# Performance work log

Measured on AMD Instinct MI355X. Metric: run time of the kernel, lower is better.

The kernel has to match this reference:

```python
import jax, jax.numpy as jnp
import numpy as np

D_HEAD = 64
KV_GROUPS = 3
KSIZE = 7


def _win_idx(L, ksize):
    # NATTEN neighborhood: window centered at i, shifted to stay in-bounds.
    start = jnp.clip(jnp.arange(L) - ksize // 2, 0, L - ksize)  # [L]
    return start[:, None] + jnp.arange(ksize)[None, :]          # [L, k]


def _natten2d(q, k, v, ksize):
    # q,k,v: [n, nh, H, W, e]; q pre-scaled.
    H, W = q.shape[2], q.shape[3]
    ih = _win_idx(H, ksize)  # [H, k]
    iw = _win_idx(W, ksize)  # [W, k]
    # gather per-query key/value windows: [n, nh, H, W, k, k, e]
    kg = k[:, :, ih[:, None, :, None], iw[None, :, None, :], :]
    vg = v[:, :, ih[:, None, :, None], iw[None, :, None, :], :]
    logits = jnp.einsum('nhije,nhijabe->nhijab', q, kg)  # [n,nh,H,W,k,k]
    n_, nh = logits.shape[:2]
    a = jax.nn.softmax(logits.reshape(n_, nh, H, W, ksize * ksize), axis=-1)
    a = a.reshape(logits.shape)
    return jnp.einsum('nhijab,nhijabe->nhije', a, vg)  # [n,nh,H,W,e]


def _to_heads(p, nh, e):
    n, h, w, _ = p.shape
    return p.reshape(n, h, w, nh, e).transpose(0, 3, 1, 2, 4)  # [n,nh,h,w,e]


def setup_inputs() -> dict:
    key = jax.random.key(0)
    k1, k2, k3 = jax.random.split(key, 3)
    x = jax.random.normal(k1, (2, 32, 32, 768), dtype=jnp.float32)
    w_qkv = jax.random.normal(k2, (1280, 768), dtype=jnp.float32) * 0.02
    w_out = jax.random.normal(k3, (768, 768), dtype=jnp.float32) * 0.02
    return {"x": x, "w_qkv": w_qkv, "w_out": w_out}


def reference(x, w_qkv, w_out):
    n, H, W, d_model = x.shape
    q_heads = d_model // D_HEAD
    kv_heads = q_heads // KV_GROUPS
    qkv = x @ w_qkv.T  # [n,H,W,1280]
    q, k, v = jnp.split(
        qkv, [q_heads * D_HEAD, (q_heads + kv_heads) * D_HEAD], axis=-1)
    q = _to_heads(q, q_heads, D_HEAD)
    k = jnp.tile(_to_heads(k, kv_heads, D_HEAD), (1, KV_GROUPS, 1, 1, 1))
    v = jnp.tile(_to_heads(v, kv_heads, D_HEAD), (1, KV_GROUPS, 1, 1, 1))
    q = q / (D_HEAD ** 0.5)
    o = _natten2d(q, k, v, KSIZE)           # [n,nh,H,W,e]
    o = o.transpose(0, 2, 3, 1, 4).reshape(n, H, W, d_model)
    return o @ w_out.T
```

## Files before the change

### kernel.cpp

```cpp
#include <hip/hip_runtime.h>
#include <hip/hip_bf16.h>


typedef __attribute__((ext_vector_type(8))) __bf16 bf16x8;
typedef __attribute__((ext_vector_type(4))) float floatx4;
typedef unsigned short u16;

__device__ inline u16 f2bf(float f) {
    union { float f; unsigned u; } v; v.f = f;
    return (u16)((v.u + 0x7fff + ((v.u >> 16) & 1)) >> 16);
}

template<int MODE>
__global__ __launch_bounds__(256) void gemm_fused(
    const void* __restrict__ Ain, const float* __restrict__ Bf,
    float* __restrict__ C, u16* __restrict__ Cb, u16* __restrict__ vT,
    int N, int K)
{
    __shared__ __align__(16) u16 As[4 * 64 * 32];
    __shared__ __align__(16) u16 Bs[4 * 64 * 32];
    const int tid = threadIdx.x;
    const int lane = tid & 63;
    const int wave = tid >> 6;
    const int bm = blockIdx.y * 64;
    const int bn = blockIdx.x * 64;
    const int qr = (wave >> 1) * 32;
    const int qc = (wave & 1) * 32;

    floatx4 acc[2][2] = {};

    const bool roleA = (wave < 2);
    const int t = tid & 127;
    const int kp = t & 15;
    const int rowg = t >> 4;
    const int bx = roleA ? bm : bn;
    u16* ldst = (roleA ? As : Bs) + (kp >> 2) * 2048 + (kp & 3) * 8;
    const bool a_is_bf16 = (MODE == 0) && roleA;
    const u16*   Xb = (const u16*)Ain;
    const float* Xf = roleA ? (const float*)Ain : Bf;

    float4 rf[8][2];
    uint4  rb[8];

    auto load_step = [&](int k0) {
        if (a_is_bf16) {
            #pragma unroll
            for (int rr = 0; rr < 8; rr++)
                rb[rr] = *(const uint4*)&Xb[(size_t)(bx + rowg * 8 + rr) * K + k0 + kp * 8];
        } else {
            #pragma unroll
            for (int rr = 0; rr < 8; rr++) {
                const float* p = &Xf[(size_t)(bx + rowg * 8 + rr) * K + k0 + kp * 8];
                rf[rr][0] = *(const float4*)p;
                rf[rr][1] = *(const float4*)(p + 4);
            }
        }
    };
    auto store_step = [&]() {
        if (a_is_bf16) {
            #pragma unroll
            for (int rr = 0; rr < 8; rr++)
                *(uint4*)&ldst[(rowg * 8 + rr) * 32] = rb[rr];
        } else {
            #pragma unroll
            for (int rr = 0; rr < 8; rr++) {
                union { u16 s[8]; uint4 v; } pk;
                pk.s[0] = f2bf(rf[rr][0].x); pk.s[1] = f2bf(rf[rr][0].y);
                pk.s[2] = f2bf(rf[rr][0].z); pk.s[3] = f2bf(rf[rr][0].w);
                pk.s[4] = f2bf(rf[rr][1].x); pk.s[5] = f2bf(rf[rr][1].y);
                pk.s[6] = f2bf(rf[rr][1].z); pk.s[7] = f2bf(rf[rr][1].w);
                *(uint4*)&ldst[(rowg * 8 + rr) * 32] = pk.v;
            }
        }
    };

    const int fr = lane & 15;
    const int fk = (lane >> 4) * 8;
    const int nk = K >> 7;

    load_step(0);
    for (int it = 0; it < nk; it++) {
        store_step();
        __syncthreads();
        if (it + 1 < nk)
            load_step((it + 1) * 128);
        #pragma unroll
        for (int kc = 0; kc < 4; kc++) {
            bf16x8 af0 = *(const bf16x8*)&As[kc * 2048 + (qr +      fr) * 32 + fk];
            bf16x8 af1 = *(const bf16x8*)&As[kc * 2048 + (qr + 16 + fr) * 32 + fk];
            bf16x8 bf0 = *(const bf16x8*)&Bs[kc * 2048 + (qc +      fr) * 32 + fk];
            bf16x8 bf1 = *(const bf16x8*)&Bs[kc * 2048 + (qc + 16 + fr) * 32 + fk];
            acc[0][0] = __builtin_amdgcn_mfma_f32_16x16x32_bf16(af0, bf0, acc[0][0], 0, 0, 0);
            acc[0][1] = __builtin_amdgcn_mfma_f32_16x16x32_bf16(af0, bf1, acc[0][1], 0, 0, 0);
            acc[1][0] = __builtin_amdgcn_mfma_f32_16x16x32_bf16(af1, bf0, acc[1][0], 0, 0, 0);
            acc[1][1] = __builtin_amdgcn_mfma_f32_16x16x32_bf16(af1, bf1, acc[1][1], 0, 0, 0);
        }
        __syncthreads();
    }

    const int cr = (lane >> 4) * 4;
    const int ccol = lane & 15;
    #pragma unroll
    for (int i = 0; i < 2; i++) {
        #pragma unroll
        for (int j = 0; j < 2; j++) {
            const int row0 = bm + qr + i * 16 + cr;
            const int col  = bn + qc + j * 16 + ccol;
            if (MODE == 0) {
                #pragma unroll
                for (int r = 0; r < 4; r++)
                    C[(size_t)(row0 + r) * N + col] = acc[i][j][r];
            } else {
                if (col < 1024) {
                    #pragma unroll
                    for (int r = 0; r < 4; r++)
                        Cb[(size_t)(row0 + r) * 1024 + col] = f2bf(acc[i][j][r]);
                } else {
                    ushort4 w;
                    w.x = f2bf(acc[i][j][0]); w.y = f2bf(acc[i][j][1]);
                    w.z = f2bf(acc[i][j][2]); w.w = f2bf(acc[i][j][3]);
                    *(ushort4*)&vT[(size_t)(col - 1024) * 2048 + row0] = w;
                }
            }
        }
    }
}

__global__ __launch_bounds__(256) void natten_mfma(
    const u16* __restrict__ qkv, const u16* __restrict__ vT,
    u16* __restrict__ o)
{
    __shared__ __align__(16) u16 Ks[224 * 72];
    __shared__ __align__(16) u16 Vs[64 * 224];
    __shared__ __align__(16) u16 Pw[4 * 512];
    const int h  = blockIdx.x;
    const int tb = blockIdx.y;
    const int g  = h & 3;
    const int batch = tb >> 4;
    const int ti = ((tb >> 2) & 3) * 8;
    const int tj = (tb & 3) * 8;
    const int wu_i = min(max(ti - 3, 0), 18);
    const int wu_j = min(max(tj - 3, 0), 18);
    const int tid = threadIdx.x, lane = tid & 63, wave = tid >> 6;
    const int pixbase = batch << 10;

    for (int c = tid; c < 1792; c += 256) {
        int n = c >> 3, seg = (c & 7) * 8;
        int a = n >> 4, b = min(n & 15, 13);
        int pix = pixbase + (wu_i + a) * 32 + wu_j + b;
        *(uint4*)&Ks[n * 72 + seg] =
            *(const uint4*)&qkv[(size_t)pix * 1024 + 768 + g * 64 + seg];
    }
    {
        const int b  = lane & 15;
        const int ar = lane >> 4;
        bool vok[4]; int voff[4];
        #pragma unroll
        for (int rr = 0; rr < 4; rr++) {
            int a = ar + rr * 4;
            vok[rr]  = (a < 14) && (b < 14);
            voff[rr] = (wu_i + a) * 32 + wu_j + b;
        }
        const u16* vsrc = &vT[(size_t)(g * 64 + wave * 16) * 2048 + pixbase];
        #pragma unroll 4
        for (int dd = 0; dd < 16; dd++) {
            #pragma unroll
            for (int rr = 0; rr < 4; rr++) {
                int a = ar + rr * 4;
                if (a < 14)
                    Vs[(wave * 16 + dd) * 224 + rr * 64 + lane] =
                        vok[rr] ? vsrc[voff[rr]] : (u16)0;
            }
            vsrc += 2048;
        }
    }
    __syncthreads();

    const int fr = lane & 15;
    const int fk = (lane >> 4) * 8;

    bf16x8 aq0, aq1;
    {
        int qq = wave * 16 + fr;
        int pixq = pixbase + (ti + (qq >> 3)) * 32 + tj + (qq & 7);
        const u16* qp = &qkv[(size_t)pixq * 1024 + h * 64];
        aq0 = *(const bf16x8*)(qp + fk);
        aq1 = *(const bf16x8*)(qp + 32 + fk);
    }

    bool colok[4]; int tlo[4], thi[4];
    #pragma unroll
    for (int r = 0; r < 4; r++) {
        int qq = wave * 16 + (lane >> 4) * 4 + r;
        int qi = ti + (qq >> 3), qj = tj + (qq & 7);
        int si = min(max(qi - 3, 0), 25);
        int sj = min(max(qj - 3, 0), 25);
        colok[r] = (fr < 14) && (wu_j + fr >= sj) && (wu_j + fr <= sj + 6);
        tlo[r] = si - wu_i; thi[r] = tlo[r] + 6;
    }

    float s[14][4];
    float mx[4] = {-1e30f, -1e30f, -1e30f, -1e30f};
    #pragma unroll
    for (int t = 0; t < 14; t++) {
        bf16x8 bk0 = *(const bf16x8*)&Ks[(t * 16 + fr) * 72 + fk];
        bf16x8 bk1 = *(const bf16x8*)&Ks[(t * 16 + fr) * 72 + 32 + fk];
        floatx4 a4 = {};
        a4 = __builtin_amdgcn_mfma_f32_16x16x32_bf16(aq0, bk0, a4, 0, 0, 0);
        a4 = __builtin_amdgcn_mfma_f32_16x16x32_bf16(aq1, bk1, a4, 0, 0, 0);
        #pragma unroll
        for (int r = 0; r < 4; r++) {
            bool v = colok[r] && (t >= tlo[r]) && (t <= thi[r]);
            s[t][r] = v ? a4[r] * 0.125f : -1e30f;
            mx[r] = fmaxf(mx[r], s[t][r]);
        }
    }
    #pragma unroll
    for (int r = 0; r < 4; r++) {
        mx[r] = fmaxf(mx[r], __shfl_xor(mx[r], 1));
        mx[r] = fmaxf(mx[r], __shfl_xor(mx[r], 2));
        mx[r] = fmaxf(mx[r], __shfl_xor(mx[r], 4));
        mx[r] = fmaxf(mx[r], __shfl_xor(mx[r], 8));
    }
    float l[4] = {0.f, 0.f, 0.f, 0.f};
    #pragma unroll
    for (int t = 0; t < 14; t++)
        #pragma unroll
        for (int r = 0; r < 4; r++) {
            float p = __expf(s[t][r] - mx[r]);
            s[t][r] = p; l[r] += p;
        }
    #pragma unroll
    for (int r = 0; r < 4; r++) {
        l[r] += __shfl_xor(l[r], 1);
        l[r] += __shfl_xor(l[r], 2);
        l[r] += __shfl_xor(l[r], 4);
        l[r] += __shfl_xor(l[r], 8);
    }
    float rinv[4];
    #pragma unroll
    for (int r = 0; r < 4; r++) rinv[r] = 1.0f / l[r];

    u16* pw = &Pw[wave * 512];
    floatx4 oacc[4] = {};
    #pragma unroll
    for (int kc = 0; kc < 7; kc++) {
        #pragma unroll
        for (int tt = 0; tt < 2; tt++) {
            int t = kc * 2 + tt;
            #pragma unroll
            for (int r = 0; r < 4; r++)
                pw[((lane >> 4) * 4 + r) * 32 + tt * 16 + fr] =
                    f2bf(s[t][r] * rinv[r]);
        }
        bf16x8 bp = *(const bf16x8*)&pw[fr * 32 + fk];
        #pragma unroll
        for (int u = 0; u < 4; u++) {
            bf16x8 av = *(const bf16x8*)&Vs[(u * 16 + fr) * 224 + kc * 32 + fk];
            oacc[u] = __builtin_amdgcn_mfma_f32_16x16x32_bf16(av, bp, oacc[u], 0, 0, 0);
        }
    }

    {
        int qq = wave * 16 + fr;
        int pixq = pixbase + (ti + (qq >> 3)) * 32 + tj + (qq & 7);
        u16* op = &o[(size_t)pixq * 768 + h * 64];
        #pragma unroll
        for (int u = 0; u < 4; u++) {
            ushort4 w;
            w.x = f2bf(oacc[u][0]); w.y = f2bf(oacc[u][1]);
            w.z = f2bf(oacc[u][2]); w.w = f2bf(oacc[u][3]);
            *(ushort4*)(op + u * 16 + (lane >> 4) * 4) = w;
        }
    }
}

extern "C" void kernel_launch(void* const* d_in, const int* in_sizes, int n_in,
                              void* d_out, int out_size, void* d_ws, size_t ws_size,
                              hipStream_t stream)
{
    const float* x     = (const float*)d_in[0];
    const float* w_qkv = (const float*)d_in[1];
    const float* w_out = (const float*)d_in[2];
    float* out = (float*)d_out;

    char* ws = (char*)d_ws;
    u16* qkvb = (u16*)ws; ws += (size_t)2048 * 1024 * 2;
    u16* vTb  = (u16*)ws; ws += (size_t)256 * 2048 * 2;
    u16* ob   = (u16*)ws;

    gemm_fused<1><<<dim3(1280 / 64, 2048 / 64), dim3(256), 0, stream>>>(
        x, w_qkv, nullptr, qkvb, vTb, 1280, 768);
    natten_mfma<<<dim3(12, 32), dim3(256), 0, stream>>>(qkvb, vTb, ob);
    gemm_fused<0><<<dim3(768 / 64, 2048 / 64), dim3(256), 0, stream>>>(
        ob, w_out, out, nullptr, nullptr, 768, 768);
}
```

Measured before the change: 121.2 us.

## Rework GEMM tile loading with all-thread staging, padded LDS and direct global-to-LDS

Replaces the split-role register-prefetch loader with a scheme where all 256 threads each convert and store one 32-wide k-chunk of a row. The fp32 operands go to LDS rows padded to 40 elements to cut bank conflicts. The bf16 A operand of the output projection is copied with global_load_lds directly into LDS, and conversion uses packed bf16x2 intrinsics. The software prefetch of the next k-step into registers is dropped, so global latency is no longer overlapped with the MFMA loop within a block and must be hidden by occupancy instead.

```diff
diff --git a/kernel.cpp b/kernel.cpp
--- a/kernel.cpp
+++ b/kernel.cpp
@@ -11,14 +11,29 @@
     return (u16)((v.u + 0x7fff + ((v.u >> 16) & 1)) >> 16);
 }
 
+__device__ inline void gl_lds16(const void* g, void* l) {
+    __builtin_amdgcn_global_load_lds(
+        (const __attribute__((address_space(1))) void*)g,
+        (__attribute__((address_space(3))) void*)l, 16, 0, 0);
+}
+
+__device__ inline uint4 pack8(float4 a, float4 b) {
+    union { __hip_bfloat162 h[4]; uint4 u; } r;
+    r.h[0] = __float22bfloat162_rn(float2{a.x, a.y});
+    r.h[1] = __float22bfloat162_rn(float2{a.z, a.w});
+    r.h[2] = __float22bfloat162_rn(float2{b.x, b.y});
+    r.h[3] = __float22bfloat162_rn(float2{b.z, b.w});
+    return r.u;
+}
+
 template<int MODE>
-__global__ __launch_bounds__(256) void gemm_fused(
+__global__ __launch_bounds__(256) void gemm_nt(
     const void* __restrict__ Ain, const float* __restrict__ Bf,
     float* __restrict__ C, u16* __restrict__ Cb, u16* __restrict__ vT,
     int N, int K)
 {
-    __shared__ __align__(16) u16 As[4 * 64 * 32];
-    __shared__ __align__(16) u16 Bs[4 * 64 * 32];
+    __shared__ __align__(16) u16 As[MODE ? 4 * 2560 : 4 * 2048];
+    __shared__ __align__(16) u16 Bs[4 * 2560];
     const int tid = threadIdx.x;
     const int lane = tid & 63;
     const int wave = tid >> 6;
@@ -29,67 +44,63 @@
 
     floatx4 acc[2][2] = {};
 
-    const bool roleA = (wave < 2);
-    const int t = tid & 127;
-    const int kp = t & 15;
-    const int rowg = t >> 4;
-    const int bx = roleA ? bm : bn;
-    u16* ldst = (roleA ? As : Bs) + (kp >> 2) * 2048 + (kp & 3) * 8;
-    const bool a_is_bf16 = (MODE == 0) && roleA;
-    const u16*   Xb = (const u16*)Ain;
-    const float* Xf = roleA ? (const float*)Ain : Bf;
-
-    float4 rf[8][2];
-    uint4  rb[8];
-
-    auto load_step = [&](int k0) {
-        if (a_is_bf16) {
-            #pragma unroll
-            for (int rr = 0; rr < 8; rr++)
-                rb[rr] = *(const uint4*)&Xb[(size_t)(bx + rowg * 8 + rr) * K + k0 + kp * 8];
-        } else {
-            #pragma unroll
-            for (int rr = 0; rr < 8; rr++) {
-                const float* p = &Xf[(size_t)(bx + rowg * 8 + rr) * K + k0 + kp * 8];
-                rf[rr][0] = *(const float4*)p;
-                rf[rr][1] = *(const float4*)(p + 4);
-            }
-        }
-    };
-    auto store_step = [&]() {
-        if (a_is_bf16) {
-            #pragma unroll
-            for (int rr = 0; rr < 8; rr++)
-                *(uint4*)&ldst[(rowg * 8 + rr) * 32] = rb[rr];
-        } else {
-            #pragma unroll
-            for (int rr = 0; rr < 8; rr++) {
-                union { u16 s[8]; uint4 v; } pk;
-                pk.s[0] = f2bf(rf[rr][0].x); pk.s[1] = f2bf(rf[rr][0].y);
-                pk.s[2] = f2bf(rf[rr][0].z); pk.s[3] = f2bf(rf[rr][0].w);
-                pk.s[4] = f2bf(rf[rr][1].x); pk.s[5] = f2bf(rf[rr][1].y);
-                pk.s[6] = f2bf(rf[rr][1].z); pk.s[7] = f2bf(rf[rr][1].w);
-                *(uint4*)&ldst[(rowg * 8 + rr) * 32] = pk.v;
-            }
-        }
-    };
+    const int srow = tid >> 2;
+    const int skc  = tid & 3;
+    const float* Bsrc = Bf + (size_t)(bn + srow) * K + skc * 32;
+    u16* Bdst = &Bs[skc * 2560 + srow * 40];
+    const float* Asrc = nullptr; u16* Adst = nullptr;
+    if (MODE) {
+        Asrc = (const float*)Ain + (size_t)(bm + srow) * K + skc * 32;
+        Adst = &As[skc * 2560 + srow * 40];
+    }
+    int gA[4], lA[4];
+    if (!MODE) {
+        #pragma unroll
+        for (int i = 0; i < 4; i++) {
+            int c = wave + 4 * i, kc = c & 3, rg = c >> 2;
+            gA[i] = (bm + rg * 16 + (lane >> 2)) * K + kc * 32 + (lane & 3) * 8;
+            lA[i] = kc * 2048 + rg * 512 + lane * 8;
+        }
+    }
 
     const int fr = lane & 15;
     const int fk = (lane >> 4) * 8;
     const int nk = K >> 7;
 
-    load_step(0);
     for (int it = 0; it < nk; it++) {
-        store_step();
+        const int k0 = it * 128;
+        {
+            const float* p = Bsrc + k0;
+            #pragma unroll
+            for (int sg = 0; sg < 4; sg++) {
+                float4 u = *(const float4*)(p + sg * 8);
+                float4 v = *(const float4*)(p + sg * 8 + 4);
+                *(uint4*)&Bdst[sg * 8] = pack8(u, v);
+            }
+        }
+        if (MODE) {
+            const float* p = Asrc + k0;
+            #pragma unroll
+            for (int sg = 0; sg < 4; sg++) {
+                float4 u = *(const float4*)(p + sg * 8);
+                float4 v = *(const float4*)(p + sg * 8 + 4);
+                *(uint4*)&Adst[sg * 8] = pack8(u, v);
+            }
+        } else {
+            const u16* Ab = (const u16*)Ain;
+            #pragma unroll
+            for (int i = 0; i < 4; i++)
+                gl_lds16(Ab + gA[i] + k0, &As[lA[i]]);
+        }
         __syncthreads();
-        if (it + 1 < nk)
-            load_step((it + 1) * 128);
         #pragma unroll
         for (int kc = 0; kc < 4; kc++) {
-            bf16x8 af0 = *(const bf16x8*)&As[kc * 2048 + (qr +      fr) * 32 + fk];
-            bf16x8 af1 = *(const bf16x8*)&As[kc * 2048 + (qr + 16 + fr) * 32 + fk];
-            bf16x8 bf0 = *(const bf16x8*)&Bs[kc * 2048 + (qc +      fr) * 32 + fk];
-            bf16x8 bf1 = *(const bf16x8*)&Bs[kc * 2048 + (qc + 16 + fr) * 32 + fk];
+            const int ap = MODE ? kc * 2560 : kc * 2048;
+            const int aw = MODE ? 40 : 32;
+            bf16x8 af0 = *(const bf16x8*)&As[ap + (qr +      fr) * aw + fk];
+            bf16x8 af1 = *(const bf16x8*)&As[ap + (qr + 16 + fr) * aw + fk];
+            bf16x8 bf0 = *(const bf16x8*)&Bs[kc * 2560 + (qc +      fr) * 40 + fk];
+            bf16x8 bf1 = *(const bf16x8*)&Bs[kc * 2560 + (qc + 16 + fr) * 40 + fk];
             acc[0][0] = __builtin_amdgcn_mfma_f32_16x16x32_bf16(af0, bf0, acc[0][0], 0, 0, 0);
             acc[0][1] = __builtin_amdgcn_mfma_f32_16x16x32_bf16(af0, bf1, acc[0][1], 0, 0, 0);
             acc[1][0] = __builtin_amdgcn_mfma_f32_16x16x32_bf16(af1, bf0, acc[1][0], 0, 0, 0);
@@ -289,9 +300,9 @@
     u16* vTb  = (u16*)ws; ws += (size_t)256 * 2048 * 2;
     u16* ob   = (u16*)ws;
 
-    gemm_fused<1><<<dim3(1280 / 64, 2048 / 64), dim3(256), 0, stream>>>(
+    gemm_nt<1><<<dim3(1280 / 64, 2048 / 64), dim3(256), 0, stream>>>(
         x, w_qkv, nullptr, qkvb, vTb, 1280, 768);
     natten_mfma<<<dim3(12, 32), dim3(256), 0, stream>>>(qkvb, vTb, ob);
-    gemm_fused<0><<<dim3(768 / 64, 2048 / 64), dim3(256), 0, stream>>>(
+    gemm_nt<0><<<dim3(768 / 64, 2048 / 64), dim3(256), 0, stream>>>(
         ob, w_out, out, nullptr, nullptr, 768, 768);
 }
```

Measured after the change: 138.5 us. 1.14x slower.
